# Kernel tuning notes

Hardware: AMD Instinct MI355X
Metric: run time of the kernel (lower is better)

## Reference

```python
import jax, jax.numpy as jnp
import numpy as np

B, CIN, COUT, K, H, W = 2, 128, 64, 64, 128, 128
BN_EPS = 1e-5


def setup_inputs() -> dict:
    key = jax.random.key(0)
    k1, k2, k3, k4 = jax.random.split(key, 4)
    x = jax.random.normal(k1, (B, CIN, H, W), dtype=jnp.float32)
    index = jax.random.randint(k2, (B, 1, H, W), 0, K)  # superpixel labels
    # kaiming_uniform(a=sqrt(5)) ~ uniform with bound sqrt(6/((1+5)*fan_in)) = 1/sqrt(fan_in)
    Wft = jax.random.uniform(k3, (CIN, COUT), dtype=jnp.float32,
                             minval=-1.0, maxval=1.0) / np.sqrt(CIN).astype(np.float32)
    Wm = jax.random.uniform(k4, (COUT, COUT), dtype=jnp.float32,
                            minval=-1.0, maxval=1.0) / np.sqrt(COUT).astype(np.float32)
    gamma = jnp.ones((COUT,), jnp.float32)
    beta = jnp.zeros((COUT,), jnp.float32)
    return {"x": x, "index": index, "Wft": Wft, "Wm": Wm, "gamma": gamma, "beta": beta}


def _gnn_forward(x, index, Wft, Wm, gamma, beta):
    # FeatureTransform: [B,Cin,H,W] -> [B,Cout,H,W]
    xt = jnp.einsum('bchw,co->bohw', x, Wft)

    idx = index[:, 0]                                   # [B,H,W]
    oh = jax.nn.one_hot(idx, K, dtype=xt.dtype)         # [B,H,W,K]

    # RegionalMeans (segment-mean over superpixels; equivalent to the
    # repeated-tensor multiply+sum in the torch code, without the 5D blowup)
    block_sum = oh.sum(axis=(1, 2))                     # [B,K]
    sums = jnp.einsum('bhwk,bohw->bko', oh, xt)         # [B,K,Cout]
    denom = block_sum + (block_sum == 0).astype(xt.dtype)
    means = sums / denom[..., None]                     # [B,K,Cout]

    # Adj: pairwise Mahalanobis distance with learned cov = Wm @ Wm.T
    cov = Wm @ Wm.T
    inv_cov = jnp.linalg.inv(cov)
    diff = means[:, :, None, :] - means[:, None, :, :]  # [B,K,K,Cout]
    q = jnp.einsum('bijc,cd,bijd->bij', diff, inv_cov, diff)
    dist = jnp.sqrt(jnp.maximum(q, 1e-12))              # clamp: diagonal q==0
    adj = jnp.exp(-dist)                                # [B,K,K]

    # GCN propagate: adjacency-weighted aggregation of region means
    adj_means = jnp.einsum('bij,bjo->bio', adj, means)  # [B,K,Cout]

    # sum_k one_hot_k * (x_rep + adj_means_k) == xt + gather(adj_means, idx)
    gathered = jnp.take_along_axis(adj_means, idx.reshape(B, -1, 1), axis=1)
    gathered = gathered.reshape(B, H, W, COUT).transpose(0, 3, 1, 2)
    features = jax.nn.relu(xt + gathered)               # [B,Cout,H,W]

    # BatchNorm2d (training-mode batch statistics, biased variance)
    mean = features.mean(axis=(0, 2, 3), keepdims=True)
    var = features.var(axis=(0, 2, 3), keepdims=True)
    out = (features - mean) / jnp.sqrt(var + BN_EPS)
    out = out * gamma[None, :, None, None] + beta[None, :, None, None]
    return out


def reference(x, index, Wft, Wm, gamma, beta):
    return _gnn_forward(x, index, Wft, Wm, gamma, beta)
```

## Files before the change

### kernel.cpp

```cpp
#include <hip/hip_runtime.h>
#include <hip/hip_bf16.h>

#define CIN   128
#define COUT  64
#define HW    16384

typedef __hip_bfloat16 bf16;

#define OFF_XT    0u
#define OFF_PS    1048576u
#define OFF_PC    2097152u
#define OFF_MEANS 2129920u
#define OFF_DIAG  2138112u
#define OFF_INV   2138240u
#define OFF_ADJM  2142336u
#define OFF_BNP   2150528u

__device__ __forceinline__ unsigned short f2bfu(float f) {
  union { bf16 h; unsigned short u; } cv; cv.h = __float2bfloat16(f); return cv.u;
}
__device__ __forceinline__ float bf2f(unsigned short u) {
  union { unsigned int i; float f; } cv; cv.i = ((unsigned int)u) << 16; return cv.f;
}

__global__ __launch_bounds__(256, 2) void k1_xt_bins_inv(
    const float* __restrict__ x, const int* __restrict__ index,
    const float* __restrict__ Wft, const float* __restrict__ Wm,
    float* __restrict__ ws)
{
  __shared__ __align__(16) float smem[16384];
  const int blk = blockIdx.x, tid = threadIdx.x;
  if (blk != 0) {
    float* xl = smem;
    float* wl = smem + 8192;
    const int eb = blk - 1;
    const int b = eb >> 8, ps = eb & 255;
    const float* xg = x + (size_t)b * CIN * HW + ps * 64;
#pragma unroll
    for (int j = 0; j < 8; ++j) {
      const int fj = j * 256 + tid;
      const int c = fj >> 4, q4 = (fj & 15) * 4;
      *(float4*)&xl[c * 64 + q4] = *(const float4*)(xg + (size_t)c * HW + q4);
      *(float4*)&wl[c * 64 + q4] = *(const float4*)(Wft + c * 64 + q4);
    }
    __syncthreads();
    const int px_grp = tid & 15, o_grp = tid >> 4;
    const int px = ps * 64 + px_grp * 4, o0 = o_grp * 4;
    float acc[16];
#pragma unroll
    for (int j = 0; j < 16; ++j) acc[j] = 0.f;
#pragma unroll 8
    for (int c = 0; c < 128; ++c) {
      const float4 xv = *(const float4*)&xl[c * 64 + px_grp * 4];
      const float4 wv = *(const float4*)&wl[c * 64 + o0];
      acc[ 0]=fmaf(xv.x,wv.x,acc[ 0]); acc[ 1]=fmaf(xv.y,wv.x,acc[ 1]);
      acc[ 2]=fmaf(xv.z,wv.x,acc[ 2]); acc[ 3]=fmaf(xv.w,wv.x,acc[ 3]);
      acc[ 4]=fmaf(xv.x,wv.y,acc[ 4]); acc[ 5]=fmaf(xv.y,wv.y,acc[ 5]);
      acc[ 6]=fmaf(xv.z,wv.y,acc[ 6]); acc[ 7]=fmaf(xv.w,wv.y,acc[ 7]);
      acc[ 8]=fmaf(xv.x,wv.z,acc[ 8]); acc[ 9]=fmaf(xv.y,wv.z,acc[ 9]);
      acc[10]=fmaf(xv.z,wv.z,acc[10]); acc[11]=fmaf(xv.w,wv.z,acc[11]);
      acc[12]=fmaf(xv.x,wv.w,acc[12]); acc[13]=fmaf(xv.y,wv.w,acc[13]);
      acc[14]=fmaf(xv.z,wv.w,acc[14]); acc[15]=fmaf(xv.w,wv.w,acc[15]);
    }
    unsigned short* xtu = (unsigned short*)(ws + OFF_XT);
#pragma unroll
    for (int oj = 0; oj < 4; ++oj) {
      ushort4 u;
      u.x = f2bfu(acc[oj*4+0]); u.y = f2bfu(acc[oj*4+1]);
      u.z = f2bfu(acc[oj*4+2]); u.w = f2bfu(acc[oj*4+3]);
      *(ushort4*)(xtu + (size_t)(b * 64 + o0 + oj) * HW + px) = u;
    }
    const int4 kv = *(const int4*)(index + b * HW + px);
    const int kk[4] = {kv.x, kv.y, kv.z, kv.w};
    __syncthreads();
    float* bins = smem;
    float* cnt  = smem + 64 * 68;
    for (int i = tid; i < 64 * 68 + 64; i += 256) smem[i] = 0.f;
    __syncthreads();
#pragma unroll
    for (int pj = 0; pj < 4; ++pj) {
      const int kb = kk[pj] * 68 + o0;
      atomicAdd(&bins[kb    ], acc[ 0 + pj]);
      atomicAdd(&bins[kb + 1], acc[ 4 + pj]);
      atomicAdd(&bins[kb + 2], acc[ 8 + pj]);
      atomicAdd(&bins[kb + 3], acc[12 + pj]);
    }
    if (o_grp == 0) {
#pragma unroll
      for (int pj = 0; pj < 4; ++pj) atomicAdd(&cnt[kk[pj]], 1.f);
    }
    __syncthreads();
    unsigned short* pb = (unsigned short*)(ws + OFF_PS) + (size_t)eb * 4096;
    {
      const int k = tid >> 2, ob = (tid & 3) * 16;
#pragma unroll
      for (int q = 0; q < 4; ++q) {
        const float4 v = *(const float4*)&bins[k * 68 + ob + q * 4];
        ushort4 u;
        u.x = f2bfu(v.x); u.y = f2bfu(v.y); u.z = f2bfu(v.z); u.w = f2bfu(v.w);
        *(ushort4*)(pb + k * 64 + ob + q * 4) = u;
      }
    }
    if (tid < 64) ws[OFF_PC + (size_t)(b * 64 + tid) * 256 + ps] = cnt[tid];
  } else {
    float* wm = smem;
    float* Rb = smem + 8192;
    float* Cb = smem + 8704;
    for (int e = tid; e < 4096; e += 256) wm[(e >> 6) * 68 + (e & 63)] = Wm[e];
    __syncthreads();
    const int ig = tid >> 4, jg = tid & 15;
    const int i0 = ig << 2, j0 = jg << 2;
    float c4[16];
#pragma unroll
    for (int q = 0; q < 16; ++q) c4[q] = 0.f;
    for (int cq = 0; cq < 64; cq += 4) {
      float4 a[4], bb[4];
#pragma unroll
      for (int ii = 0; ii < 4; ++ii) a[ii]  = *(const float4*)&wm[(i0+ii)*68 + cq];
#pragma unroll
      for (int jj = 0; jj < 4; ++jj) bb[jj] = *(const float4*)&wm[(j0+jj)*68 + cq];
#pragma unroll
      for (int ii = 0; ii < 4; ++ii)
#pragma unroll
        for (int jj = 0; jj < 4; ++jj)
          c4[ii*4+jj] = fmaf(a[ii].x, bb[jj].x, fmaf(a[ii].y, bb[jj].y,
                        fmaf(a[ii].z, bb[jj].z, fmaf(a[ii].w, bb[jj].w, c4[ii*4+jj]))));
    }
    __syncthreads();
    __builtin_amdgcn_s_setprio(3);
    int buf = 0;
#pragma unroll 1
    for (int p = 0; p < 16; ++p) {
      const int P = p << 2;
      float* Rp = Rb + buf * 256;
      float* Cp = Cb + buf * 256;
      if (ig == p) {
#pragma unroll
        for (int r = 0; r < 4; ++r) {
          float4 t; t.x = c4[r*4+0]; t.y = c4[r*4+1]; t.z = c4[r*4+2]; t.w = c4[r*4+3];
          *(float4*)&Rp[r * 64 + j0] = t;
        }
      }
      if (jg == p) {
#pragma unroll
        for (int ii = 0; ii < 4; ++ii) {
          float4 t; t.x = c4[ii*4+0]; t.y = c4[ii*4+1]; t.z = c4[ii*4+2]; t.w = c4[ii*4+3];
          *(float4*)&Cp[(i0 + ii) * 4] = t;
        }
      }
      __syncthreads();
      float dd[16], cc[16], rr[16];
#pragma unroll
      for (int r = 0; r < 4; ++r) *(float4*)&dd[r * 4] = *(const float4*)&Rp[r * 64 + P];
#pragma unroll
      for (int ii = 0; ii < 4; ++ii) *(float4*)&cc[ii * 4] = *(const float4*)&Cp[(i0 + ii) * 4];
#pragma unroll
      for (int r = 0; r < 4; ++r) *(float4*)&rr[r * 4] = *(const float4*)&Rp[r * 64 + j0];
#pragma unroll
      for (int k = 0; k < 4; ++k) {
        const float rp = __builtin_amdgcn_rcpf(dd[k * 4 + k]);
        float ai[4], s[4];
#pragma unroll
        for (int j = 0; j < 4; ++j) s[j] = dd[k * 4 + j];
#pragma unroll
        for (int i = 0; i < 4; ++i) ai[i] = (i == k) ? (rp - 1.0f) : (-dd[i * 4 + k] * rp);
#pragma unroll
        for (int i = 0; i < 4; ++i)
#pragma unroll
          for (int j = 0; j < 4; ++j) dd[i * 4 + j] = fmaf(ai[i], s[j], dd[i * 4 + j]);
#pragma unroll
        for (int i = 0; i < 4; ++i) dd[i * 4 + k] = (i == k) ? rp : ai[i];
      }
      float T[16];
#pragma unroll
      for (int ii = 0; ii < 4; ++ii)
#pragma unroll
        for (int c = 0; c < 4; ++c) {
          float t = cc[ii*4+0] * dd[0*4+c];
          t = fmaf(cc[ii*4+1], dd[1*4+c], t);
          t = fmaf(cc[ii*4+2], dd[2*4+c], t);
          t = fmaf(cc[ii*4+3], dd[3*4+c], t);
          T[ii*4+c] = t;
        }
      if (ig == p && jg == p) {
#pragma unroll
        for (int q = 0; q < 16; ++q) c4[q] = dd[q];
      } else if (ig == p) {
#pragma unroll
        for (int r = 0; r < 4; ++r)
#pragma unroll
          for (int jj = 0; jj < 4; ++jj) {
            float t = dd[r*4+0] * rr[0*4+jj];
            t = fmaf(dd[r*4+1], rr[1*4+jj], t);
            t = fmaf(dd[r*4+2], rr[2*4+jj], t);
            t = fmaf(dd[r*4+3], rr[3*4+jj], t);
            c4[r*4+jj] = t;
          }
      } else if (jg == p) {
#pragma unroll
        for (int q = 0; q < 16; ++q) c4[q] = -T[q];
      } else {
#pragma unroll
        for (int ii = 0; ii < 4; ++ii)
#pragma unroll
          for (int jj = 0; jj < 4; ++jj) {
            float t = c4[ii*4+jj];
            t = fmaf(-T[ii*4+0], rr[0*4+jj], t);
            t = fmaf(-T[ii*4+1], rr[1*4+jj], t);
            t = fmaf(-T[ii*4+2], rr[2*4+jj], t);
            t = fmaf(-T[ii*4+3], rr[3*4+jj], t);
            c4[ii*4+jj] = t;
          }
      }
      buf ^= 1;
    }
    __builtin_amdgcn_s_setprio(0);
#pragma unroll
    for (int ii = 0; ii < 4; ++ii)
#pragma unroll
      for (int jj = 0; jj < 4; ++jj)
        ws[OFF_INV + (size_t)(i0 + ii) * 64 + j0 + jj] = c4[ii*4+jj];
  }
}

__global__ __launch_bounds__(1024) void k15_means_diag(float* __restrict__ ws)
{
  __shared__ float red[1024];
  __shared__ float lds_c[4];
  __shared__ float lds_m[64];
  const int blk = blockIdx.x, t = threadIdx.x;
  const int b = blk >> 6, k = blk & 63;
  const int o = t & 63, chunk = t >> 6;
  const unsigned short* psu = (const unsigned short*)(ws + OFF_PS);
  float s = 0.f;
#pragma unroll
  for (int i = 0; i < 16; ++i) {
    const int slab = chunk * 16 + i;
    s += bf2f(psu[(size_t)(b * 256 + slab) * 4096 + k * 64 + o]);
  }
  red[chunk * 64 + o] = s;
  float cv = 0.f;
  if (t < 256) cv = ws[OFF_PC + (size_t)(b * 64 + k) * 256 + t];
#pragma unroll
  for (int m = 32; m; m >>= 1) cv += __shfl_xor(cv, m, 64);
  if (t < 256 && (t & 63) == 0) lds_c[t >> 6] = cv;
  __syncthreads();
  if (t < 64) {
    float m_raw = 0.f;
#pragma unroll
    for (int ch = 0; ch < 16; ++ch) m_raw += red[ch * 64 + o];
    const float cnt = lds_c[0] + lds_c[1] + lds_c[2] + lds_c[3];
    const float denom = cnt + ((cnt == 0.f) ? 1.f : 0.f);
    const float m = m_raw / denom;
    ws[OFF_MEANS + (size_t)(b * 64 + k) * 64 + o] = m;
    lds_m[o] = m;
    float inner = 0.f;
#pragma unroll 8
    for (int d = 0; d < 64; ++d) inner = fmaf(ws[OFF_INV + d * 64 + o], lds_m[d], inner);
    float p = m * inner;
#pragma unroll
    for (int mm = 32; mm; mm >>= 1) p += __shfl_xor(p, mm, 64);
    if (o == 0) ws[OFF_DIAG + b * 64 + k] = p;
  }
}

__global__ __launch_bounds__(256) void k2_adj(float* __restrict__ ws)
{
  __shared__ __align__(16) float means_s[64 * 68];
  __shared__ __align__(16) float inv_s[64 * 68];
  __shared__ __align__(16) float T_s[8 * 68];
  __shared__ __align__(16) float adj_s[8 * 68];
  __shared__ float diag_s[64];
  const int b = blockIdx.x >> 3;
  const int i0 = (blockIdx.x & 7) << 3;
  const int t = threadIdx.x;
  const float* mg = ws + OFF_MEANS + b * 4096;
  for (int e = t; e < 4096; e += 256) means_s[(e >> 6) * 68 + (e & 63)] = mg[e];
  const float* ig = ws + OFF_INV;
  for (int e = t; e < 4096; e += 256) inv_s[(e >> 6) * 68 + (e & 63)] = ig[e];
  if (t < 64) diag_s[t] = ws[OFF_DIAG + b * 64 + t];
  __syncthreads();
  if (t < 128) {
    const int i = t >> 4, d0 = (t & 15) << 2;
    float4 acc = {0.f, 0.f, 0.f, 0.f};
    for (int c = 0; c < 64; ++c) {
      const float mv = means_s[(i0 + i) * 68 + c];
      const float4 iv = *(const float4*)&inv_s[c * 68 + d0];
      acc.x = fmaf(mv, iv.x, acc.x); acc.y = fmaf(mv, iv.y, acc.y);
      acc.z = fmaf(mv, iv.z, acc.z); acc.w = fmaf(mv, iv.w, acc.w);
    }
    *(float4*)&T_s[i * 68 + d0] = acc;
  }
  __syncthreads();
  {
    const int i = t >> 5, jb = t & 31;
#pragma unroll
    for (int jj = 0; jj < 2; ++jj) {
      const int j = jb + (jj << 5);
      float4 p4 = {0.f, 0.f, 0.f, 0.f};
      for (int dq = 0; dq < 64; dq += 4) {
        const float4 tv = *(const float4*)&T_s[i * 68 + dq];
        const float4 mv = *(const float4*)&means_s[j * 68 + dq];
        p4.x = fmaf(tv.x, mv.x, p4.x); p4.y = fmaf(tv.y, mv.y, p4.y);
        p4.z = fmaf(tv.z, mv.z, p4.z); p4.w = fmaf(tv.w, mv.w, p4.w);
      }
      const float p = (p4.x + p4.y) + (p4.z + p4.w);
      const float q = diag_s[i0 + i] + diag_s[j] - 2.f * p;
      adj_s[i * 68 + j] = __expf(-sqrtf(fmaxf(q, 1e-12f)));
    }
  }
  __syncthreads();
  if (t < 128) {
    const int i = t >> 4, oq = (t & 15) << 2;
    float4 am = {0.f, 0.f, 0.f, 0.f};
    for (int j = 0; j < 64; ++j) {
      const float av = adj_s[i * 68 + j];
      const float4 mv = *(const float4*)&means_s[j * 68 + oq];
      am.x = fmaf(av, mv.x, am.x); am.y = fmaf(av, mv.y, am.y);
      am.z = fmaf(av, mv.z, am.z); am.w = fmaf(av, mv.w, am.w);
    }
    *(float4*)(ws + OFF_ADJM + (size_t)(b * 64 + i0 + i) * 64 + oq) = am;
  }
}

__global__ __launch_bounds__(256) void k3_bnstats(const int* __restrict__ index,
                                                  float* __restrict__ ws)
{
  __shared__ float am_s[128];
  __shared__ float red[4];
  const int blk = blockIdx.x, t = threadIdx.x;
  const int b = blk >> 8, oc = (blk >> 3) & 31, tile = blk & 7;
  const int o0 = oc * 2;
  if (t < 128) am_s[t] = ws[OFF_ADJM + (size_t)(b * 64 + (t >> 1)) * 64 + o0 + (t & 1)];
  if (t < 4) red[t] = 0.f;
  __syncthreads();
  const int lane = t & 63, w = t >> 6;
  const unsigned short* xtu = (const unsigned short*)(ws + OFF_XT);
  float s0 = 0.f, s1 = 0.f, q0 = 0.f, q1 = 0.f;
#pragma unroll
  for (int q = 0; q < 2; ++q) {
    const int px = tile * 2048 + (w * 2 + q) * 256 + lane * 4;
    const int4 kv = *(const int4*)(index + b * HW + px);
    const ushort4 u0 = *(const ushort4*)(xtu + (size_t)(b * 64 + o0    ) * HW + px);
    const ushort4 u1 = *(const ushort4*)(xtu + (size_t)(b * 64 + o0 + 1) * HW + px);
    const int kk[4] = {kv.x, kv.y, kv.z, kv.w};
    const float x0[4] = {bf2f(u0.x), bf2f(u0.y), bf2f(u0.z), bf2f(u0.w)};
    const float x1[4] = {bf2f(u1.x), bf2f(u1.y), bf2f(u1.z), bf2f(u1.w)};
#pragma unroll
    for (int j = 0; j < 4; ++j) {
      const float2 am = *(const float2*)&am_s[kk[j] * 2];
      const float f0 = fmaxf(x0[j] + am.x, 0.f);
      const float f1 = fmaxf(x1[j] + am.y, 0.f);
      s0 += f0; q0 = fmaf(f0, f0, q0);
      s1 += f1; q1 = fmaf(f1, f1, q1);
    }
  }
#pragma unroll
  for (int m = 1; m < 64; m <<= 1) {
    s0 += __shfl_xor(s0, m, 64); s1 += __shfl_xor(s1, m, 64);
    q0 += __shfl_xor(q0, m, 64); q1 += __shfl_xor(q1, m, 64);
  }
  if (lane == 0) {
    atomicAdd(&red[0], s0); atomicAdd(&red[1], s1);
    atomicAdd(&red[2], q0); atomicAdd(&red[3], q1);
  }
  __syncthreads();
  if (t == 0) {
    float4 v; v.x = red[0]; v.y = red[1]; v.z = red[2]; v.w = red[3];
    *(float4*)(ws + OFF_BNP + (size_t)(oc * 16 + b * 8 + tile) * 4) = v;
  }
}

__global__ __launch_bounds__(256) void k4_out(const int* __restrict__ index,
    const float* __restrict__ gamma, const float* __restrict__ beta,
    const float* __restrict__ ws, float* __restrict__ out)
{
  __shared__ float am_s[128];
  __shared__ float4 tmp[16];
  __shared__ float sc_s[2], sh_s[2];
  const int blk = blockIdx.x, t = threadIdx.x;
  const int b = blk >> 8, oc = (blk >> 3) & 31, tile = blk & 7;
  const int o0 = oc * 2;
  if (t < 128) am_s[t] = ws[OFF_ADJM + (size_t)(b * 64 + (t >> 1)) * 64 + o0 + (t & 1)];
  if (t < 16) tmp[t] = *(const float4*)(ws + OFF_BNP + (size_t)(oc * 16 + t) * 4);
  if (t < 2) {
    float s = 0.f, qq = 0.f;
#pragma unroll
    for (int i = 0; i < 16; ++i) {
      const float4 v = tmp[i];
      s  += (t == 0) ? v.x : v.y;
      qq += (t == 0) ? v.z : v.w;
    }
    const float mean = s * (1.f / 32768.f);
    const float var  = qq * (1.f / 32768.f) - mean * mean;
    const float sc = gamma[o0 + t] * rsqrtf(var + 1e-5f);
    sc_s[t] = sc;
    sh_s[t] = fmaf(-mean, sc, beta[o0 + t]);
  }
  __syncthreads();
  const int lane = t & 63, w = t >> 6;
  const unsigned short* xtu = (const unsigned short*)(ws + OFF_XT);
  const float c0 = sc_s[0], c1 = sc_s[1], h0 = sh_s[0], h1 = sh_s[1];
#pragma unroll
  for (int q = 0; q < 2; ++q) {
    const int px = tile * 2048 + (w * 2 + q) * 256 + lane * 4;
    const int4 kv = *(const int4*)(index + b * HW + px);
    const ushort4 u0 = *(const ushort4*)(xtu + (size_t)(b * 64 + o0    ) * HW + px);
    const ushort4 u1 = *(const ushort4*)(xtu + (size_t)(b * 64 + o0 + 1) * HW + px);
    const int kk[4] = {kv.x, kv.y, kv.z, kv.w};
    const float x0[4] = {bf2f(u0.x), bf2f(u0.y), bf2f(u0.z), bf2f(u0.w)};
    const float x1[4] = {bf2f(u1.x), bf2f(u1.y), bf2f(u1.z), bf2f(u1.w)};
    float4 o4a, o4b;
    float* oa = (float*)&o4a; float* ob = (float*)&o4b;
#pragma unroll
    for (int j = 0; j < 4; ++j) {
      const float2 am = *(const float2*)&am_s[kk[j] * 2];
      oa[j] = fmaf(fmaxf(x0[j] + am.x, 0.f), c0, h0);
      ob[j] = fmaf(fmaxf(x1[j] + am.y, 0.f), c1, h1);
    }
    *(float4*)(out + (size_t)(b * 64 + o0    ) * HW + px) = o4a;
    *(float4*)(out + (size_t)(b * 64 + o0 + 1) * HW + px) = o4b;
  }
}

extern "C" void kernel_launch(void* const* d_in, const int* in_sizes, int n_in,
                              void* d_out, int out_size, void* d_ws, size_t ws_size,
                              hipStream_t stream) {
  const float* x     = (const float*)d_in[0];
  const int*   index = (const int*)d_in[1];
  const float* Wft   = (const float*)d_in[2];
  const float* Wm    = (const float*)d_in[3];
  const float* gamma = (const float*)d_in[4];
  const float* beta  = (const float*)d_in[5];
  float* ws  = (float*)d_ws;
  float* out = (float*)d_out;

  k1_xt_bins_inv<<<513, 256, 0, stream>>>(x, index, Wft, Wm, ws);
  k15_means_diag<<<128, 1024, 0, stream>>>(ws);
  k2_adj<<<16, 256, 0, stream>>>(ws);
  k3_bnstats<<<512, 256, 0, stream>>>(index, ws);
  k4_out<<<512, 256, 0, stream>>>(index, gamma, beta, ws, out);
}
```

Measured before the change: 120.1 us.

## Fuse five kernels into one cooperative persistent kernel with grid syncs

Merges the xt/bins/inverse, means, adjacency, BN-stats and output kernels into a single cooperative kernel of 512 blocks separated by grid.sync barriers. The goal is to remove four kernel launch gaps and the tail drain between small dependent stages. The diagonal Mahalanobis term now comes from the adjacency stage instead of the means stage, and the matrix inverse runs on block 511 after the main pass instead of in a separate block. The kernel relies on all 512 blocks being co-resident, and the small middle stages keep most blocks idle at each barrier.

```diff
diff --git a/kernel.cpp b/kernel.cpp
--- a/kernel.cpp
+++ b/kernel.cpp
@@ -1,5 +1,8 @@
 #include <hip/hip_runtime.h>
 #include <hip/hip_bf16.h>
+#include <hip/hip_cooperative_groups.h>
+
+namespace cg = cooperative_groups;
 
 #define CIN   128
 #define COUT  64
@@ -11,7 +14,6 @@
 #define OFF_PS    1048576u
 #define OFF_PC    2097152u
 #define OFF_MEANS 2129920u
-#define OFF_DIAG  2138112u
 #define OFF_INV   2138240u
 #define OFF_ADJM  2142336u
 #define OFF_BNP   2150528u
@@ -23,18 +25,20 @@
   union { unsigned int i; float f; } cv; cv.i = ((unsigned int)u) << 16; return cv.f;
 }
 
-__global__ __launch_bounds__(256, 2) void k1_xt_bins_inv(
+__global__ __launch_bounds__(256, 2) void k_mega(
     const float* __restrict__ x, const int* __restrict__ index,
     const float* __restrict__ Wft, const float* __restrict__ Wm,
-    float* __restrict__ ws)
+    const float* __restrict__ gamma, const float* __restrict__ beta,
+    float* __restrict__ ws, float* __restrict__ out)
 {
   __shared__ __align__(16) float smem[16384];
+  cg::grid_group grid = cg::this_grid();
   const int blk = blockIdx.x, tid = threadIdx.x;
-  if (blk != 0) {
+
+  {
     float* xl = smem;
     float* wl = smem + 8192;
-    const int eb = blk - 1;
-    const int b = eb >> 8, ps = eb & 255;
+    const int b = blk >> 8, ps = blk & 255;
     const float* xg = x + (size_t)b * CIN * HW + ps * 64;
 #pragma unroll
     for (int j = 0; j < 8; ++j) {
@@ -90,7 +94,7 @@
       for (int pj = 0; pj < 4; ++pj) atomicAdd(&cnt[kk[pj]], 1.f);
     }
     __syncthreads();
-    unsigned short* pb = (unsigned short*)(ws + OFF_PS) + (size_t)eb * 4096;
+    unsigned short* pb = (unsigned short*)(ws + OFF_PS) + (size_t)blk * 4096;
     {
       const int k = tid >> 2, ob = (tid & 3) * 16;
 #pragma unroll
@@ -102,7 +106,35 @@
       }
     }
     if (tid < 64) ws[OFF_PC + (size_t)(b * 64 + tid) * 256 + ps] = cnt[tid];
-  } else {
+  }
+
+  grid.sync();
+
+  if (blk < 128) {
+    float* red   = smem;
+    float* lds_c = smem + 256;
+    const int b = blk >> 6, k = blk & 63;
+    const int o = tid & 63, chunk = tid >> 6;
+    const unsigned short* psu = (const unsigned short*)(ws + OFF_PS);
+    float s = 0.f;
+#pragma unroll 8
+    for (int i = 0; i < 64; ++i) {
+      const int slab = chunk * 64 + i;
+      s += bf2f(psu[(size_t)(b * 256 + slab) * 4096 + k * 64 + o]);
+    }
+    red[chunk * 64 + o] = s;
+    float cv = ws[OFF_PC + (size_t)(b * 64 + k) * 256 + tid];
+#pragma unroll
+    for (int m = 32; m; m >>= 1) cv += __shfl_xor(cv, m, 64);
+    if ((tid & 63) == 0) lds_c[tid >> 6] = cv;
+    __syncthreads();
+    if (tid < 64) {
+      const float m_raw = red[o] + red[64 + o] + red[128 + o] + red[192 + o];
+      const float cnt = lds_c[0] + lds_c[1] + lds_c[2] + lds_c[3];
+      const float denom = cnt + ((cnt == 0.f) ? 1.f : 0.f);
+      ws[OFF_MEANS + (size_t)(b * 64 + k) * 64 + o] = m_raw / denom;
+    }
+  } else if (blk == 511) {
     float* wm = smem;
     float* Rb = smem + 8192;
     float* Cb = smem + 8704;
@@ -221,205 +253,175 @@
       for (int jj = 0; jj < 4; ++jj)
         ws[OFF_INV + (size_t)(i0 + ii) * 64 + j0 + jj] = c4[ii*4+jj];
   }
-}
-
-__global__ __launch_bounds__(1024) void k15_means_diag(float* __restrict__ ws)
-{
-  __shared__ float red[1024];
-  __shared__ float lds_c[4];
-  __shared__ float lds_m[64];
-  const int blk = blockIdx.x, t = threadIdx.x;
-  const int b = blk >> 6, k = blk & 63;
-  const int o = t & 63, chunk = t >> 6;
-  const unsigned short* psu = (const unsigned short*)(ws + OFF_PS);
-  float s = 0.f;
-#pragma unroll
-  for (int i = 0; i < 16; ++i) {
-    const int slab = chunk * 16 + i;
-    s += bf2f(psu[(size_t)(b * 256 + slab) * 4096 + k * 64 + o]);
+
+  grid.sync();
+
+  if (blk < 16) {
+    float* means_s = smem;
+    float* inv_s   = smem + 4352;
+    float* Tf_s    = smem + 8704;
+    float* adj_s   = smem + 13056;
+    float* diag_s  = smem + 13600;
+    const int b = blk >> 3;
+    const int i0 = (blk & 7) << 3;
+    const float* mg = ws + OFF_MEANS + b * 4096;
+    for (int e = tid; e < 4096; e += 256) means_s[(e >> 6) * 68 + (e & 63)] = mg[e];
+    const float* ig = ws + OFF_INV;
+    for (int e = tid; e < 4096; e += 256) inv_s[(e >> 6) * 68 + (e & 63)] = ig[e];
+    __syncthreads();
+    {
+      const int i = tid >> 2, d0 = (tid & 3) << 4;
+      float4 acc4[4];
+#pragma unroll
+      for (int q = 0; q < 4; ++q) acc4[q] = (float4){0.f, 0.f, 0.f, 0.f};
+      for (int c = 0; c < 64; ++c) {
+        const float mv = means_s[i * 68 + c];
+#pragma unroll
+        for (int q = 0; q < 4; ++q) {
+          const float4 iv = *(const float4*)&inv_s[c * 68 + d0 + q * 4];
+          acc4[q].x = fmaf(mv, iv.x, acc4[q].x); acc4[q].y = fmaf(mv, iv.y, acc4[q].y);
+          acc4[q].z = fmaf(mv, iv.z, acc4[q].z); acc4[q].w = fmaf(mv, iv.w, acc4[q].w);
+        }
+      }
+#pragma unroll
+      for (int q = 0; q < 4; ++q) *(float4*)&Tf_s[i * 68 + d0 + q * 4] = acc4[q];
+    }
+    __syncthreads();
+    if (tid < 64) {
+      float dv = 0.f;
+      for (int dq = 0; dq < 64; dq += 4) {
+        const float4 tv = *(const float4*)&Tf_s[tid * 68 + dq];
+        const float4 mv = *(const float4*)&means_s[tid * 68 + dq];
+        dv = fmaf(tv.x, mv.x, fmaf(tv.y, mv.y, fmaf(tv.z, mv.z, fmaf(tv.w, mv.w, dv))));
+      }
+      diag_s[tid] = dv;
+    }
+    __syncthreads();
+    {
+      const int i = tid >> 5, jb = tid & 31;
+#pragma unroll
+      for (int jj = 0; jj < 2; ++jj) {
+        const int j = jb + (jj << 5);
+        float4 p4 = {0.f, 0.f, 0.f, 0.f};
+        for (int dq = 0; dq < 64; dq += 4) {
+          const float4 tv = *(const float4*)&Tf_s[(i0 + i) * 68 + dq];
+          const float4 mv = *(const float4*)&means_s[j * 68 + dq];
+          p4.x = fmaf(tv.x, mv.x, p4.x); p4.y = fmaf(tv.y, mv.y, p4.y);
+          p4.z = fmaf(tv.z, mv.z, p4.z); p4.w = fmaf(tv.w, mv.w, p4.w);
+        }
+        const float p = (p4.x + p4.y) + (p4.z + p4.w);
+        const float q = diag_s[i0 + i] + diag_s[j] - 2.f * p;
+        adj_s[i * 68 + j] = __expf(-sqrtf(fmaxf(q, 1e-12f)));
+      }
+    }
+    __syncthreads();
+    if (tid < 128) {
+      const int i = tid >> 4, oq = (tid & 15) << 2;
+      float4 am = {0.f, 0.f, 0.f, 0.f};
+      for (int j = 0; j < 64; ++j) {
+        const float av = adj_s[i * 68 + j];
+        const float4 mv = *(const float4*)&means_s[j * 68 + oq];
+        am.x = fmaf(av, mv.x, am.x); am.y = fmaf(av, mv.y, am.y);
+        am.z = fmaf(av, mv.z, am.z); am.w = fmaf(av, mv.w, am.w);
+      }
+      *(float4*)(ws + OFF_ADJM + (size_t)(b * 64 + i0 + i) * 64 + oq) = am;
+    }
   }
-  red[chunk * 64 + o] = s;
-  float cv = 0.f;
-  if (t < 256) cv = ws[OFF_PC + (size_t)(b * 64 + k) * 256 + t];
-#pragma unroll
-  for (int m = 32; m; m >>= 1) cv += __shfl_xor(cv, m, 64);
-  if (t < 256 && (t & 63) == 0) lds_c[t >> 6] = cv;
-  __syncthreads();
-  if (t < 64) {
-    float m_raw = 0.f;
-#pragma unroll
-    for (int ch = 0; ch < 16; ++ch) m_raw += red[ch * 64 + o];
-    const float cnt = lds_c[0] + lds_c[1] + lds_c[2] + lds_c[3];
-    const float denom = cnt + ((cnt == 0.f) ? 1.f : 0.f);
-    const float m = m_raw / denom;
-    ws[OFF_MEANS + (size_t)(b * 64 + k) * 64 + o] = m;
-    lds_m[o] = m;
-    float inner = 0.f;
-#pragma unroll 8
-    for (int d = 0; d < 64; ++d) inner = fmaf(ws[OFF_INV + d * 64 + o], lds_m[d], inner);
-    float p = m * inner;
-#pragma unroll
-    for (int mm = 32; mm; mm >>= 1) p += __shfl_xor(p, mm, 64);
-    if (o == 0) ws[OFF_DIAG + b * 64 + k] = p;
+
+  grid.sync();
+
+  const int b45 = blk >> 8, oc = (blk >> 3) & 31, tile = blk & 7;
+  const int o0 = oc * 2;
+  {
+    float* am_s = smem;
+    float* red  = smem + 128;
+    if (tid < 128) am_s[tid] = ws[OFF_ADJM + (size_t)(b45 * 64 + (tid >> 1)) * 64 + o0 + (tid & 1)];
+    if (tid < 4) red[tid] = 0.f;
+    __syncthreads();
+    const int lane = tid & 63, w = tid >> 6;
+    const unsigned short* xtu = (const unsigned short*)(ws + OFF_XT);
+    float s0 = 0.f, s1 = 0.f, q0 = 0.f, q1 = 0.f;
+#pragma unroll
+    for (int q = 0; q < 2; ++q) {
+      const int px = tile * 2048 + (w * 2 + q) * 256 + lane * 4;
+      const int4 kv = *(const int4*)(index + b45 * HW + px);
+      const ushort4 u0 = *(const ushort4*)(xtu + (size_t)(b45 * 64 + o0    ) * HW + px);
+      const ushort4 u1 = *(const ushort4*)(xtu + (size_t)(b45 * 64 + o0 + 1) * HW + px);
+      const int kk[4] = {kv.x, kv.y, kv.z, kv.w};
+      const float x0[4] = {bf2f(u0.x), bf2f(u0.y), bf2f(u0.z), bf2f(u0.w)};
+      const float x1[4] = {bf2f(u1.x), bf2f(u1.y), bf2f(u1.z), bf2f(u1.w)};
+#pragma unroll
+      for (int j = 0; j < 4; ++j) {
+        const float2 am = *(const float2*)&am_s[kk[j] * 2];
+        const float f0 = fmaxf(x0[j] + am.x, 0.f);
+        const float f1 = fmaxf(x1[j] + am.y, 0.f);
+        s0 += f0; q0 = fmaf(f0, f0, q0);
+        s1 += f1; q1 = fmaf(f1, f1, q1);
+      }
+    }
+#pragma unroll
+    for (int m = 1; m < 64; m <<= 1) {
+      s0 += __shfl_xor(s0, m, 64); s1 += __shfl_xor(s1, m, 64);
+      q0 += __shfl_xor(q0, m, 64); q1 += __shfl_xor(q1, m, 64);
+    }
+    if (lane == 0) {
+      atomicAdd(&red[0], s0); atomicAdd(&red[1], s1);
+      atomicAdd(&red[2], q0); atomicAdd(&red[3], q1);
+    }
+    __syncthreads();
+    if (tid == 0) {
+      float4 v; v.x = red[0]; v.y = red[1]; v.z = red[2]; v.w = red[3];
+      *(float4*)(ws + OFF_BNP + (size_t)(oc * 16 + b45 * 8 + tile) * 4) = v;
+    }
   }
-}
-
-__global__ __launch_bounds__(256) void k2_adj(float* __restrict__ ws)
-{
-  __shared__ __align__(16) float means_s[64 * 68];
-  __shared__ __align__(16) float inv_s[64 * 68];
-  __shared__ __align__(16) float T_s[8 * 68];
-  __shared__ __align__(16) float adj_s[8 * 68];
-  __shared__ float diag_s[64];
-  const int b = blockIdx.x >> 3;
-  const int i0 = (blockIdx.x & 7) << 3;
-  const int t = threadIdx.x;
-  const float* mg = ws + OFF_MEANS + b * 4096;
-  for (int e = t; e < 4096; e += 256) means_s[(e >> 6) * 68 + (e & 63)] = mg[e];
-  const float* ig = ws + OFF_INV;
-  for (int e = t; e < 4096; e += 256) inv_s[(e >> 6) * 68 + (e & 63)] = ig[e];
-  if (t < 64) diag_s[t] = ws[OFF_DIAG + b * 64 + t];
-  __syncthreads();
-  if (t < 128) {
-    const int i = t >> 4, d0 = (t & 15) << 2;
-    float4 acc = {0.f, 0.f, 0.f, 0.f};
-    for (int c = 0; c < 64; ++c) {
-      const float mv = means_s[(i0 + i) * 68 + c];
-      const float4 iv = *(const float4*)&inv_s[c * 68 + d0];
-      acc.x = fmaf(mv, iv.x, acc.x); acc.y = fmaf(mv, iv.y, acc.y);
-      acc.z = fmaf(mv, iv.z, acc.z); acc.w = fmaf(mv, iv.w, acc.w);
-    }
-    *(float4*)&T_s[i * 68 + d0] = acc;
-  }
-  __syncthreads();
+
+  grid.sync();
+
   {
-    const int i = t >> 5, jb = t & 31;
-#pragma unroll
-    for (int jj = 0; jj < 2; ++jj) {
-      const int j = jb + (jj << 5);
-      float4 p4 = {0.f, 0.f, 0.f, 0.f};
-      for (int dq = 0; dq < 64; dq += 4) {
-        const float4 tv = *(const float4*)&T_s[i * 68 + dq];
-        const float4 mv = *(const float4*)&means_s[j * 68 + dq];
-        p4.x = fmaf(tv.x, mv.x, p4.x); p4.y = fmaf(tv.y, mv.y, p4.y);
-        p4.z = fmaf(tv.z, mv.z, p4.z); p4.w = fmaf(tv.w, mv.w, p4.w);
-      }
-      const float p = (p4.x + p4.y) + (p4.z + p4.w);
-      const float q = diag_s[i0 + i] + diag_s[j] - 2.f * p;
-      adj_s[i * 68 + j] = __expf(-sqrtf(fmaxf(q, 1e-12f)));
-    }
-  }
-  __syncthreads();
-  if (t < 128) {
-    const int i = t >> 4, oq = (t & 15) << 2;
-    float4 am = {0.f, 0.f, 0.f, 0.f};
-    for (int j = 0; j < 64; ++j) {
-      const float av = adj_s[i * 68 + j];
-      const float4 mv = *(const float4*)&means_s[j * 68 + oq];
-      am.x = fmaf(av, mv.x, am.x); am.y = fmaf(av, mv.y, am.y);
-      am.z = fmaf(av, mv.z, am.z); am.w = fmaf(av, mv.w, am.w);
-    }
-    *(float4*)(ws + OFF_ADJM + (size_t)(b * 64 + i0 + i) * 64 + oq) = am;
-  }
-}
-
-__global__ __launch_bounds__(256) void k3_bnstats(const int* __restrict__ index,
-                                                  float* __restrict__ ws)
-{
-  __shared__ float am_s[128];
-  __shared__ float red[4];
-  const int blk = blockIdx.x, t = threadIdx.x;
-  const int b = blk >> 8, oc = (blk >> 3) & 31, tile = blk & 7;
-  const int o0 = oc * 2;
-  if (t < 128) am_s[t] = ws[OFF_ADJM + (size_t)(b * 64 + (t >> 1)) * 64 + o0 + (t & 1)];
-  if (t < 4) red[t] = 0.f;
-  __syncthreads();
-  const int lane = t & 63, w = t >> 6;
-  const unsigned short* xtu = (const unsigned short*)(ws + OFF_XT);
-  float s0 = 0.f, s1 = 0.f, q0 = 0.f, q1 = 0.f;
-#pragma unroll
-  for (int q = 0; q < 2; ++q) {
-    const int px = tile * 2048 + (w * 2 + q) * 256 + lane * 4;
-    const int4 kv = *(const int4*)(index + b * HW + px);
-    const ushort4 u0 = *(const ushort4*)(xtu + (size_t)(b * 64 + o0    ) * HW + px);
-    const ushort4 u1 = *(const ushort4*)(xtu + (size_t)(b * 64 + o0 + 1) * HW + px);
-    const int kk[4] = {kv.x, kv.y, kv.z, kv.w};
-    const float x0[4] = {bf2f(u0.x), bf2f(u0.y), bf2f(u0.z), bf2f(u0.w)};
-    const float x1[4] = {bf2f(u1.x), bf2f(u1.y), bf2f(u1.z), bf2f(u1.w)};
-#pragma unroll
-    for (int j = 0; j < 4; ++j) {
-      const float2 am = *(const float2*)&am_s[kk[j] * 2];
-      const float f0 = fmaxf(x0[j] + am.x, 0.f);
-      const float f1 = fmaxf(x1[j] + am.y, 0.f);
-      s0 += f0; q0 = fmaf(f0, f0, q0);
-      s1 += f1; q1 = fmaf(f1, f1, q1);
-    }
-  }
-#pragma unroll
-  for (int m = 1; m < 64; m <<= 1) {
-    s0 += __shfl_xor(s0, m, 64); s1 += __shfl_xor(s1, m, 64);
-    q0 += __shfl_xor(q0, m, 64); q1 += __shfl_xor(q1, m, 64);
-  }
-  if (lane == 0) {
-    atomicAdd(&red[0], s0); atomicAdd(&red[1], s1);
-    atomicAdd(&red[2], q0); atomicAdd(&red[3], q1);
-  }
-  __syncthreads();
-  if (t == 0) {
-    float4 v; v.x = red[0]; v.y = red[1]; v.z = red[2]; v.w = red[3];
-    *(float4*)(ws + OFF_BNP + (size_t)(oc * 16 + b * 8 + tile) * 4) = v;
-  }
-}
-
-__global__ __launch_bounds__(256) void k4_out(const int* __restrict__ index,
-    const float* __restrict__ gamma, const float* __restrict__ beta,
-    const float* __restrict__ ws, float* __restrict__ out)
-{
-  __shared__ float am_s[128];
-  __shared__ float4 tmp[16];
-  __shared__ float sc_s[2], sh_s[2];
-  const int blk = blockIdx.x, t = threadIdx.x;
-  const int b = blk >> 8, oc = (blk >> 3) & 31, tile = blk & 7;
-  const int o0 = oc * 2;
-  if (t < 128) am_s[t] = ws[OFF_ADJM + (size_t)(b * 64 + (t >> 1)) * 64 + o0 + (t & 1)];
-  if (t < 16) tmp[t] = *(const float4*)(ws + OFF_BNP + (size_t)(oc * 16 + t) * 4);
-  if (t < 2) {
-    float s = 0.f, qq = 0.f;
-#pragma unroll
-    for (int i = 0; i < 16; ++i) {
-      const float4 v = tmp[i];
-      s  += (t == 0) ? v.x : v.y;
-      qq += (t == 0) ? v.z : v.w;
-    }
-    const float mean = s * (1.f / 32768.f);
-    const float var  = qq * (1.f / 32768.f) - mean * mean;
-    const float sc = gamma[o0 + t] * rsqrtf(var + 1e-5f);
-    sc_s[t] = sc;
-    sh_s[t] = fmaf(-mean, sc, beta[o0 + t]);
-  }
-  __syncthreads();
-  const int lane = t & 63, w = t >> 6;
-  const unsigned short* xtu = (const unsigned short*)(ws + OFF_XT);
-  const float c0 = sc_s[0], c1 = sc_s[1], h0 = sh_s[0], h1 = sh_s[1];
-#pragma unroll
-  for (int q = 0; q < 2; ++q) {
-    const int px = tile * 2048 + (w * 2 + q) * 256 + lane * 4;
-    const int4 kv = *(const int4*)(index + b * HW + px);
-    const ushort4 u0 = *(const ushort4*)(xtu + (size_t)(b * 64 + o0    ) * HW + px);
-    const ushort4 u1 = *(const ushort4*)(xtu + (size_t)(b * 64 + o0 + 1) * HW + px);
-    const int kk[4] = {kv.x, kv.y, kv.z, kv.w};
-    const float x0[4] = {bf2f(u0.x), bf2f(u0.y), bf2f(u0.z), bf2f(u0.w)};
-    const float x1[4] = {bf2f(u1.x), bf2f(u1.y), bf2f(u1.z), bf2f(u1.w)};
-    float4 o4a, o4b;
-    float* oa = (float*)&o4a; float* ob = (float*)&o4b;
-#pragma unroll
-    for (int j = 0; j < 4; ++j) {
-      const float2 am = *(const float2*)&am_s[kk[j] * 2];
-      oa[j] = fmaf(fmaxf(x0[j] + am.x, 0.f), c0, h0);
-      ob[j] = fmaf(fmaxf(x1[j] + am.y, 0.f), c1, h1);
-    }
-    *(float4*)(out + (size_t)(b * 64 + o0    ) * HW + px) = o4a;
-    *(float4*)(out + (size_t)(b * 64 + o0 + 1) * HW + px) = o4b;
+    float*  am_s = smem;
+    float4* tmp  = (float4*)(smem + 128);
+    float*  sc_s = smem + 192;
+    float*  sh_s = smem + 194;
+    if (tid < 128) am_s[tid] = ws[OFF_ADJM + (size_t)(b45 * 64 + (tid >> 1)) * 64 + o0 + (tid & 1)];
+    if (tid < 16) tmp[tid] = *(const float4*)(ws + OFF_BNP + (size_t)(oc * 16 + tid) * 4);
+    if (tid < 2) {
+      float s = 0.f, qq = 0.f;
+#pragma unroll
+      for (int i = 0; i < 16; ++i) {
+        const float4 v = tmp[i];
+        s  += (tid == 0) ? v.x : v.y;
+        qq += (tid == 0) ? v.z : v.w;
+      }
+      const float mean = s * (1.f / 32768.f);
+      const float var  = qq * (1.f / 32768.f) - mean * mean;
+      const float sc = gamma[o0 + tid] * rsqrtf(var + 1e-5f);
+      sc_s[tid] = sc;
+      sh_s[tid] = fmaf(-mean, sc, beta[o0 + tid]);
+    }
+    __syncthreads();
+    const int lane = tid & 63, w = tid >> 6;
+    const unsigned short* xtu = (const unsigned short*)(ws + OFF_XT);
+    const float c0 = sc_s[0], c1 = sc_s[1], h0 = sh_s[0], h1 = sh_s[1];
+#pragma unroll
+    for (int q = 0; q < 2; ++q) {
+      const int px = tile * 2048 + (w * 2 + q) * 256 + lane * 4;
+      const int4 kv = *(const int4*)(index + b45 * HW + px);
+      const ushort4 u0 = *(const ushort4*)(xtu + (size_t)(b45 * 64 + o0    ) * HW + px);
+      const ushort4 u1 = *(const ushort4*)(xtu + (size_t)(b45 * 64 + o0 + 1) * HW + px);
+      const int kk[4] = {kv.x, kv.y, kv.z, kv.w};
+      const float x0[4] = {bf2f(u0.x), bf2f(u0.y), bf2f(u0.z), bf2f(u0.w)};
+      const float x1[4] = {bf2f(u1.x), bf2f(u1.y), bf2f(u1.z), bf2f(u1.w)};
+      float4 o4a, o4b;
+      float* oa = (float*)&o4a; float* ob = (float*)&o4b;
+#pragma unroll
+      for (int j = 0; j < 4; ++j) {
+        const float2 am = *(const float2*)&am_s[kk[j] * 2];
+        oa[j] = fmaf(fmaxf(x0[j] + am.x, 0.f), c0, h0);
+        ob[j] = fmaf(fmaxf(x1[j] + am.y, 0.f), c1, h1);
+      }
+      *(float4*)(out + (size_t)(b45 * 64 + o0    ) * HW + px) = o4a;
+      *(float4*)(out + (size_t)(b45 * 64 + o0 + 1) * HW + px) = o4b;
+    }
   }
 }
 
@@ -435,9 +437,7 @@
   float* ws  = (float*)d_ws;
   float* out = (float*)d_out;
 
-  k1_xt_bins_inv<<<513, 256, 0, stream>>>(x, index, Wft, Wm, ws);
-  k15_means_diag<<<128, 1024, 0, stream>>>(ws);
-  k2_adj<<<16, 256, 0, stream>>>(ws);
-  k3_bnstats<<<512, 256, 0, stream>>>(index, ws);
-  k4_out<<<512, 256, 0, stream>>>(index, gamma, beta, ws, out);
+  void* args[] = {(void*)&x, (void*)&index, (void*)&Wft, (void*)&Wm,
+                  (void*)&gamma, (void*)&beta, (void*)&ws, (void*)&out};
+  hipLaunchCooperativeKernel((const void*)k_mega, dim3(512), dim3(256), args, 0, stream);
 }
```

Result: slower. 344.8 us (+187.2%).

## Fuse region-mean and adjacency kernels into first kernel with atomic spin barriers

Applied to the files above, without the earlier changes.

Merges the region-mean/diagonal and adjacency kernels into the first kernel. Extra blocks spin on global atomic counters until the projection/binning blocks and the covariance-inverse block have published their results. This removes two kernel launches and their inter-kernel gaps. The means stage is also reshaped from 1024 to 256 threads per block, and the priority boost on the inverse block is dropped. The scheme relies on in-order block dispatch and on block 0 resetting the counters before any increment, which risks a race or deadlock.

```diff
diff --git a/kernel.cpp b/kernel.cpp
--- a/kernel.cpp
+++ b/kernel.cpp
@@ -15,6 +15,7 @@
 #define OFF_INV   2138240u
 #define OFF_ADJM  2142336u
 #define OFF_BNP   2150528u
+#define OFF_SYNC  2152576u
 
 __device__ __forceinline__ unsigned short f2bfu(float f) {
   union { bf16 h; unsigned short u; } cv; cv.h = __float2bfloat16(f); return cv.u;
@@ -22,15 +23,21 @@
 __device__ __forceinline__ float bf2f(unsigned short u) {
   union { unsigned int i; float f; } cv; cv.i = ((unsigned int)u) << 16; return cv.f;
 }
-
-__global__ __launch_bounds__(256, 2) void k1_xt_bins_inv(
+__device__ __forceinline__ void spin_until(int* p, int target) {
+  while (__hip_atomic_load(p, __ATOMIC_ACQUIRE, __HIP_MEMORY_SCOPE_AGENT) != target)
+    __builtin_amdgcn_s_sleep(1);
+}
+
+__global__ __launch_bounds__(256, 2) void k1_fused(
     const float* __restrict__ x, const int* __restrict__ index,
     const float* __restrict__ Wft, const float* __restrict__ Wm,
     float* __restrict__ ws)
 {
   __shared__ __align__(16) float smem[16384];
   const int blk = blockIdx.x, tid = threadIdx.x;
-  if (blk != 0) {
+  int* sync = (int*)(ws + OFF_SYNC);
+
+  if (blk >= 1 && blk <= 512) {
     float* xl = smem;
     float* wl = smem + 8192;
     const int eb = blk - 1;
@@ -102,7 +109,13 @@
       }
     }
     if (tid < 64) ws[OFF_PC + (size_t)(b * 64 + tid) * 256 + ps] = cnt[tid];
-  } else {
+    __syncthreads();
+    if (tid == 0) { __threadfence(); atomicAdd(&sync[0], 1); }
+
+  } else if (blk == 0) {
+    if (tid == 0) {
+      atomicExch(&sync[0], 0); atomicExch(&sync[1], 0); atomicExch(&sync[2], 0);
+    }
     float* wm = smem;
     float* Rb = smem + 8192;
     float* Cb = smem + 8704;
@@ -127,7 +140,6 @@
                         fmaf(a[ii].z, bb[jj].z, fmaf(a[ii].w, bb[jj].w, c4[ii*4+jj]))));
     }
     __syncthreads();
-    __builtin_amdgcn_s_setprio(3);
     int buf = 0;
 #pragma unroll 1
     for (int p = 0; p < 16; ++p) {
@@ -214,112 +226,112 @@
       }
       buf ^= 1;
     }
-    __builtin_amdgcn_s_setprio(0);
 #pragma unroll
     for (int ii = 0; ii < 4; ++ii)
 #pragma unroll
       for (int jj = 0; jj < 4; ++jj)
         ws[OFF_INV + (size_t)(i0 + ii) * 64 + j0 + jj] = c4[ii*4+jj];
-  }
-}
-
-__global__ __launch_bounds__(1024) void k15_means_diag(float* __restrict__ ws)
-{
-  __shared__ float red[1024];
-  __shared__ float lds_c[4];
-  __shared__ float lds_m[64];
-  const int blk = blockIdx.x, t = threadIdx.x;
-  const int b = blk >> 6, k = blk & 63;
-  const int o = t & 63, chunk = t >> 6;
-  const unsigned short* psu = (const unsigned short*)(ws + OFF_PS);
-  float s = 0.f;
-#pragma unroll
-  for (int i = 0; i < 16; ++i) {
-    const int slab = chunk * 16 + i;
-    s += bf2f(psu[(size_t)(b * 256 + slab) * 4096 + k * 64 + o]);
-  }
-  red[chunk * 64 + o] = s;
-  float cv = 0.f;
-  if (t < 256) cv = ws[OFF_PC + (size_t)(b * 64 + k) * 256 + t];
-#pragma unroll
-  for (int m = 32; m; m >>= 1) cv += __shfl_xor(cv, m, 64);
-  if (t < 256 && (t & 63) == 0) lds_c[t >> 6] = cv;
-  __syncthreads();
-  if (t < 64) {
-    float m_raw = 0.f;
-#pragma unroll
-    for (int ch = 0; ch < 16; ++ch) m_raw += red[ch * 64 + o];
-    const float cnt = lds_c[0] + lds_c[1] + lds_c[2] + lds_c[3];
-    const float denom = cnt + ((cnt == 0.f) ? 1.f : 0.f);
-    const float m = m_raw / denom;
-    ws[OFF_MEANS + (size_t)(b * 64 + k) * 64 + o] = m;
-    lds_m[o] = m;
-    float inner = 0.f;
+    __syncthreads();
+    if (tid == 0) { __threadfence(); atomicExch(&sync[2], 777); }
+
+  } else if (blk <= 640) {
+    if (tid == 0) { spin_until(&sync[0], 512); spin_until(&sync[2], 777); }
+    __syncthreads();
+    float* red   = smem;
+    float* lds_c = smem + 256;
+    float* lds_m = smem + 260;
+    const int rb = blk - 513;
+    const int b = rb >> 6, k = rb & 63;
+    const int o = tid & 63, chunk = tid >> 6;
+    const unsigned short* psu = (const unsigned short*)(ws + OFF_PS);
+    float s = 0.f;
 #pragma unroll 8
-    for (int d = 0; d < 64; ++d) inner = fmaf(ws[OFF_INV + d * 64 + o], lds_m[d], inner);
-    float p = m * inner;
-#pragma unroll
-    for (int mm = 32; mm; mm >>= 1) p += __shfl_xor(p, mm, 64);
-    if (o == 0) ws[OFF_DIAG + b * 64 + k] = p;
-  }
-}
-
-__global__ __launch_bounds__(256) void k2_adj(float* __restrict__ ws)
-{
-  __shared__ __align__(16) float means_s[64 * 68];
-  __shared__ __align__(16) float inv_s[64 * 68];
-  __shared__ __align__(16) float T_s[8 * 68];
-  __shared__ __align__(16) float adj_s[8 * 68];
-  __shared__ float diag_s[64];
-  const int b = blockIdx.x >> 3;
-  const int i0 = (blockIdx.x & 7) << 3;
-  const int t = threadIdx.x;
-  const float* mg = ws + OFF_MEANS + b * 4096;
-  for (int e = t; e < 4096; e += 256) means_s[(e >> 6) * 68 + (e & 63)] = mg[e];
-  const float* ig = ws + OFF_INV;
-  for (int e = t; e < 4096; e += 256) inv_s[(e >> 6) * 68 + (e & 63)] = ig[e];
-  if (t < 64) diag_s[t] = ws[OFF_DIAG + b * 64 + t];
-  __syncthreads();
-  if (t < 128) {
-    const int i = t >> 4, d0 = (t & 15) << 2;
-    float4 acc = {0.f, 0.f, 0.f, 0.f};
-    for (int c = 0; c < 64; ++c) {
-      const float mv = means_s[(i0 + i) * 68 + c];
-      const float4 iv = *(const float4*)&inv_s[c * 68 + d0];
-      acc.x = fmaf(mv, iv.x, acc.x); acc.y = fmaf(mv, iv.y, acc.y);
-      acc.z = fmaf(mv, iv.z, acc.z); acc.w = fmaf(mv, iv.w, acc.w);
-    }
-    *(float4*)&T_s[i * 68 + d0] = acc;
-  }
-  __syncthreads();
-  {
-    const int i = t >> 5, jb = t & 31;
-#pragma unroll
-    for (int jj = 0; jj < 2; ++jj) {
-      const int j = jb + (jj << 5);
-      float4 p4 = {0.f, 0.f, 0.f, 0.f};
-      for (int dq = 0; dq < 64; dq += 4) {
-        const float4 tv = *(const float4*)&T_s[i * 68 + dq];
-        const float4 mv = *(const float4*)&means_s[j * 68 + dq];
-        p4.x = fmaf(tv.x, mv.x, p4.x); p4.y = fmaf(tv.y, mv.y, p4.y);
-        p4.z = fmaf(tv.z, mv.z, p4.z); p4.w = fmaf(tv.w, mv.w, p4.w);
-      }
-      const float p = (p4.x + p4.y) + (p4.z + p4.w);
-      const float q = diag_s[i0 + i] + diag_s[j] - 2.f * p;
-      adj_s[i * 68 + j] = __expf(-sqrtf(fmaxf(q, 1e-12f)));
-    }
-  }
-  __syncthreads();
-  if (t < 128) {
-    const int i = t >> 4, oq = (t & 15) << 2;
-    float4 am = {0.f, 0.f, 0.f, 0.f};
-    for (int j = 0; j < 64; ++j) {
-      const float av = adj_s[i * 68 + j];
-      const float4 mv = *(const float4*)&means_s[j * 68 + oq];
-      am.x = fmaf(av, mv.x, am.x); am.y = fmaf(av, mv.y, am.y);
-      am.z = fmaf(av, mv.z, am.z); am.w = fmaf(av, mv.w, am.w);
-    }
-    *(float4*)(ws + OFF_ADJM + (size_t)(b * 64 + i0 + i) * 64 + oq) = am;
+    for (int i = 0; i < 64; ++i) {
+      const int slab = chunk * 64 + i;
+      s += bf2f(psu[(size_t)(b * 256 + slab) * 4096 + k * 64 + o]);
+    }
+    red[chunk * 64 + o] = s;
+    float cv = ws[OFF_PC + (size_t)(b * 64 + k) * 256 + tid];
+#pragma unroll
+    for (int m = 32; m; m >>= 1) cv += __shfl_xor(cv, m, 64);
+    if ((tid & 63) == 0) lds_c[tid >> 6] = cv;
+    __syncthreads();
+    if (tid < 64) {
+      const float m_raw = red[o] + red[64 + o] + red[128 + o] + red[192 + o];
+      const float cnt = lds_c[0] + lds_c[1] + lds_c[2] + lds_c[3];
+      const float denom = cnt + ((cnt == 0.f) ? 1.f : 0.f);
+      const float m = m_raw / denom;
+      ws[OFF_MEANS + (size_t)(b * 64 + k) * 64 + o] = m;
+      lds_m[o] = m;
+      float inner = 0.f;
+#pragma unroll 8
+      for (int d = 0; d < 64; ++d) inner = fmaf(ws[OFF_INV + d * 64 + o], lds_m[d], inner);
+      float p = m * inner;
+#pragma unroll
+      for (int mm = 32; mm; mm >>= 1) p += __shfl_xor(p, mm, 64);
+      if (o == 0) ws[OFF_DIAG + b * 64 + k] = p;
+    }
+    __syncthreads();
+    if (tid == 0) { __threadfence(); atomicAdd(&sync[1], 1); }
+
+  } else {
+    if (tid == 0) spin_until(&sync[1], 128);
+    __syncthreads();
+    float* means_s = smem;
+    float* inv_s   = smem + 4352;
+    float* T_s     = smem + 8704;
+    float* adj_s   = smem + 9248;
+    float* diag_s  = smem + 9792;
+    const int ab = blk - 641;
+    const int b = ab >> 3;
+    const int i0 = (ab & 7) << 3;
+    const float* mg = ws + OFF_MEANS + b * 4096;
+    for (int e = tid; e < 4096; e += 256) means_s[(e >> 6) * 68 + (e & 63)] = mg[e];
+    const float* ig = ws + OFF_INV;
+    for (int e = tid; e < 4096; e += 256) inv_s[(e >> 6) * 68 + (e & 63)] = ig[e];
+    if (tid < 64) diag_s[tid] = ws[OFF_DIAG + b * 64 + tid];
+    __syncthreads();
+    if (tid < 128) {
+      const int i = tid >> 4, d0 = (tid & 15) << 2;
+      float4 acc = {0.f, 0.f, 0.f, 0.f};
+      for (int c = 0; c < 64; ++c) {
+        const float mv = means_s[(i0 + i) * 68 + c];
+        const float4 iv = *(const float4*)&inv_s[c * 68 + d0];
+        acc.x = fmaf(mv, iv.x, acc.x); acc.y = fmaf(mv, iv.y, acc.y);
+        acc.z = fmaf(mv, iv.z, acc.z); acc.w = fmaf(mv, iv.w, acc.w);
+      }
+      *(float4*)&T_s[i * 68 + d0] = acc;
+    }
+    __syncthreads();
+    {
+      const int i = tid >> 5, jb = tid & 31;
+#pragma unroll
+      for (int jj = 0; jj < 2; ++jj) {
+        const int j = jb + (jj << 5);
+        float4 p4 = {0.f, 0.f, 0.f, 0.f};
+        for (int dq = 0; dq < 64; dq += 4) {
+          const float4 tv = *(const float4*)&T_s[i * 68 + dq];
+          const float4 mv = *(const float4*)&means_s[j * 68 + dq];
+          p4.x = fmaf(tv.x, mv.x, p4.x); p4.y = fmaf(tv.y, mv.y, p4.y);
+          p4.z = fmaf(tv.z, mv.z, p4.z); p4.w = fmaf(tv.w, mv.w, p4.w);
+        }
+        const float p = (p4.x + p4.y) + (p4.z + p4.w);
+        const float q = diag_s[i0 + i] + diag_s[j] - 2.f * p;
+        adj_s[i * 68 + j] = __expf(-sqrtf(fmaxf(q, 1e-12f)));
+      }
+    }
+    __syncthreads();
+    if (tid < 128) {
+      const int i = tid >> 4, oq = (tid & 15) << 2;
+      float4 am = {0.f, 0.f, 0.f, 0.f};
+      for (int j = 0; j < 64; ++j) {
+        const float av = adj_s[i * 68 + j];
+        const float4 mv = *(const float4*)&means_s[j * 68 + oq];
+        am.x = fmaf(av, mv.x, am.x); am.y = fmaf(av, mv.y, am.y);
+        am.z = fmaf(av, mv.z, am.z); am.w = fmaf(av, mv.w, am.w);
+      }
+      *(float4*)(ws + OFF_ADJM + (size_t)(b * 64 + i0 + i) * 64 + oq) = am;
+    }
   }
 }
 
@@ -435,9 +447,7 @@
   float* ws  = (float*)d_ws;
   float* out = (float*)d_out;
 
-  k1_xt_bins_inv<<<513, 256, 0, stream>>>(x, index, Wft, Wm, ws);
-  k15_means_diag<<<128, 1024, 0, stream>>>(ws);
-  k2_adj<<<16, 256, 0, stream>>>(ws);
+  k1_fused<<<657, 256, 0, stream>>>(x, index, Wft, Wm, ws);
   k3_bnstats<<<512, 256, 0, stream>>>(index, ws);
   k4_out<<<512, 256, 0, stream>>>(index, gamma, beta, ws, out);
 }
```

Measured after the change: 158.2 us. 1.32x slower.
